# Optimization experiments

Measured on AMD Instinct MI355X. Metric: run time of the kernel, lower is better.

The kernel has to match this reference:

```python
import jax, jax.numpy as jnp
import numpy as np

B = 131072
SD, AD, HID = 24, 8, 32
NH = SD + AD            # n_heads = 32
UNITS = HID * NH        # 1024


def _xavier(k, shape):
    fan_in, fan_out = shape[-2], shape[-1]
    lim = float(np.sqrt(6.0 / (fan_in + fan_out)))
    return jax.random.uniform(k, shape, jnp.float32, -lim, lim)


def setup_inputs() -> dict:
    key = jax.random.key(0)
    ks = jax.random.split(key, 8)
    return dict(
        state=jax.random.normal(ks[0], (B, SD), jnp.float32),
        action=jax.random.normal(ks[1], (B, AD), jnp.float32),
        # ripple layer 1: per-head Linear(NH -> HID), gate logits init 0 (init_prob=0.5)
        W1=_xavier(ks[2], (NH, NH, HID)), b1=jnp.zeros((NH, HID), jnp.float32), g1=jnp.zeros((NH,), jnp.float32),
        # ripple layer 2: per-head Linear(UNITS -> HID)
        W2=_xavier(ks[3], (NH, UNITS, HID)), b2=jnp.zeros((NH, HID), jnp.float32), g2=jnp.zeros((NH,), jnp.float32),
        # q_network
        Wq1=_xavier(ks[4], (UNITS, 256)), bq1=jnp.zeros((256,), jnp.float32),
        ln1_g=jnp.ones((256,), jnp.float32), ln1_b=jnp.zeros((256,), jnp.float32),
        Wq2=_xavier(ks[5], (256, 128)), bq2=jnp.zeros((128,), jnp.float32),
        ln2_g=jnp.ones((128,), jnp.float32), ln2_b=jnp.zeros((128,), jnp.float32),
        Wq3=_xavier(ks[6], (128, 1)), bq3=jnp.zeros((1,), jnp.float32),
    )


def _ripple(x, W, b, g):
    # x: [B, D]; W: [H, D, K]; per-head linear + tanh, scaled by per-head sigmoid gate
    h = jnp.tanh(jnp.einsum('bd,hdk->bhk', x, W) + b[None])  # [B, H, K]
    h = h * jax.nn.sigmoid(g)[None, :, None]
    return h.reshape(x.shape[0], -1)  # [B, H*K]


def _ln(x, g, b, eps=1e-5):
    mu = jnp.mean(x, -1, keepdims=True)
    var = jnp.mean((x - mu) ** 2, -1, keepdims=True)
    return (x - mu) * jax.lax.rsqrt(var + eps) * g + b


def reference(state, action, W1, b1, g1, W2, b2, g2,
              Wq1, bq1, ln1_g, ln1_b, Wq2, bq2, ln2_g, ln2_b, Wq3, bq3):
    sa = jnp.concatenate([state, action], axis=1)          # [B, SD+AD]
    x = _ripple(sa, W1, b1, g1)                            # [B, UNITS]
    x = _ripple(x, W2, b2, g2)                             # [B, UNITS]
    h = jax.nn.relu(_ln(x @ Wq1 + bq1, ln1_g, ln1_b))      # [B, 256] (dropout = eval identity)
    h = jax.nn.relu(_ln(h @ Wq2 + bq2, ln2_g, ln2_b))      # [B, 128]
    return h @ Wq3 + bq3                                   # [B, 1]
```

## Files before the change

### kernel.cpp

```cpp
#include <hip/hip_runtime.h>
#include <hip/hip_bf16.h>

typedef _Float16 f16x8 __attribute__((ext_vector_type(8)));
typedef _Float16 f16x4 __attribute__((ext_vector_type(4)));
typedef float f32x4 __attribute__((ext_vector_type(4)));

__device__ __forceinline__ float tanh_fast(float x) {
  float e = __expf(2.0f * x);
  return 1.0f - 2.0f * __builtin_amdgcn_rcpf(e + 1.0f);
}
__device__ __forceinline__ float sigmoid_fast(float x) {
  return __builtin_amdgcn_rcpf(1.0f + __expf(-x));
}

__global__ __launch_bounds__(256) void prep_weights(
    const float* __restrict__ W1, const float* __restrict__ W2,
    const float* __restrict__ Wq1, const float* __restrict__ Wq2,
    _Float16* __restrict__ V1p, _Float16* __restrict__ V2p,
    _Float16* __restrict__ T1p, _Float16* __restrict__ T2p) {
  __shared__ float S[32 * 33];
  int b = blockIdx.x, t = threadIdx.x;
  if (b < 2624) {
    const float* in; _Float16* out; int N, nc0, tile;
    if (b < 2048) {
      int h = b >> 6, rem = b & 63, ntl = rem >> 5, kt = rem & 31;
      in = W2 + (size_t)h * 32768 + (size_t)kt * 32 * 32;
      N = 32; nc0 = ntl * 16;
      out = V2p; tile = (h * 2 + ntl) * 32 + kt;
    } else if (b < 2560) {
      int i = b - 2048, nt = i >> 5, kt = i & 31;
      in = Wq1 + (size_t)kt * 32 * 256; N = 256; nc0 = nt * 16;
      out = T1p; tile = nt * 32 + kt;
    } else {
      int i = b - 2560, nt = i >> 3, kt = i & 7;
      in = Wq2 + (size_t)kt * 32 * 128; N = 128; nc0 = nt * 16;
      out = T2p; tile = nt * 8 + kt;
    }
    if (t < 128) {
      int r = t >> 2, c4 = (t & 3) * 4;
      const float4 v = *(const float4*)(in + (size_t)r * N + nc0 + c4);
      S[r * 17 + c4 + 0] = v.x; S[r * 17 + c4 + 1] = v.y;
      S[r * 17 + c4 + 2] = v.z; S[r * 17 + c4 + 3] = v.w;
    }
    __syncthreads();
    if (t < 128) {
      int w2 = t >> 6, l = t & 63, q = l >> 4, l15 = l & 15;
      f16x4 o;
#pragma unroll
      for (int jj = 0; jj < 4; ++jj)
        o[jj] = (_Float16)S[(q * 8 + w2 * 4 + jj) * 17 + l15];
      *(f16x4*)(out + (size_t)tile * 512 + l * 8 + w2 * 4) = o;
    }
  } else {
    int h = b - 2624;
    const float* in = W1 + h * 1024;
    int cc = t & 31, rr8 = t >> 5;
#pragma unroll
    for (int p = 0; p < 4; ++p) {
      int r = rr8 + p * 8;
      S[cc * 33 + r] = in[r * 32 + cc];
    }
    __syncthreads();
    if (t < 128) {
      int ntl = t >> 6, l = t & 63, q = l >> 4, l15 = l & 15;
      f16x8 o;
#pragma unroll
      for (int j = 0; j < 8; ++j)
        o[j] = (_Float16)S[(ntl * 16 + l15) * 33 + q * 8 + j];
      *(f16x8*)(V1p + (size_t)(h * 2 + ntl) * 512 + l * 8) = o;
    }
  }
}

__global__ __launch_bounds__(256) void k1_ripple1(
    const float* __restrict__ state, const float* __restrict__ action,
    const _Float16* __restrict__ v1p, const float* __restrict__ b1,
    const float* __restrict__ g1, _Float16* __restrict__ x1p, int gro) {
  __shared__ __align__(16) _Float16 SM[128 * 68];
  int bn = blockIdx.x, bm = blockIdx.y;
  int t = threadIdx.x, w = t >> 6, l = t & 63, q = l >> 4, l15 = l & 15;
  int n0 = bn * 128, m0 = bm * 128;

  {
    int r = t >> 1, half = t & 1;
    size_t grow = (size_t)(gro + m0 + r);
    float v[16];
    if (half == 0) {
      const float4* sp = (const float4*)(state + grow * 24);
      ((float4*)v)[0] = sp[0]; ((float4*)v)[1] = sp[1];
      ((float4*)v)[2] = sp[2]; ((float4*)v)[3] = sp[3];
    } else {
      const float4* sp = (const float4*)(state + grow * 24 + 16);
      ((float4*)v)[0] = sp[0]; ((float4*)v)[1] = sp[1];
      const float4* ap = (const float4*)(action + grow * 8);
      ((float4*)v)[2] = ap[0]; ((float4*)v)[3] = ap[1];
    }
    f16x8 h0, h1;
#pragma unroll
    for (int j = 0; j < 8; ++j) { h0[j] = (_Float16)v[j]; h1[j] = (_Float16)v[8 + j]; }
    *(f16x8*)&SM[r * 40 + half * 16] = h0;
    *(f16x8*)&SM[r * 40 + half * 16 + 8] = h1;
  }
  __syncthreads();

  int wr = w >> 1, wc = w & 1;
  f16x8 af[4], bf[4];
#pragma unroll
  for (int mi = 0; mi < 4; ++mi)
    af[mi] = *(const f16x8*)&SM[(wr * 64 + mi * 16 + l15) * 40 + q * 8];
#pragma unroll
  for (int ni = 0; ni < 4; ++ni)
    bf[ni] = *(const f16x8*)(v1p + (size_t)(bn * 8 + wc * 4 + ni) * 512 + l * 8);

  f32x4 acc[4][4] = {};
#pragma unroll
  for (int mi = 0; mi < 4; ++mi)
#pragma unroll
    for (int ni = 0; ni < 4; ++ni)
      acc[mi][ni] = __builtin_amdgcn_mfma_f32_16x16x32_f16(af[mi], bf[ni], acc[mi][ni], 0, 0, 0);

  for (int p = 0; p < 2; ++p) {
    __syncthreads();
    if (wc == p) {
#pragma unroll
      for (int ni = 0; ni < 4; ++ni) {
        int col = n0 + p * 64 + ni * 16 + l15;
        float sg = sigmoid_fast(g1[col >> 5]);
        float bias = b1[col];
#pragma unroll
        for (int mi = 0; mi < 4; ++mi)
#pragma unroll
          for (int r = 0; r < 4; ++r) {
            int rl = wr * 64 + mi * 16 + q * 4 + r;
            SM[rl * 68 + ni * 16 + l15] = (_Float16)(tanh_fast(acc[mi][ni][r] + bias) * sg);
          }
      }
    }
    __syncthreads();
#pragma unroll
    for (int i = 0; i < 4; ++i) {
      int c = t + i * 256;
      int kcL = c >> 9, rt = (c >> 6) & 7, ll = c & 63;
      int qq = ll >> 4, ll15 = ll & 15;
      int base = (rt * 16 + ll15) * 68 + kcL * 32 + qq * 8;
      union { f16x8 v; f16x4 h[2]; } u;
      u.h[0] = *(const f16x4*)&SM[base];
      u.h[1] = *(const f16x4*)&SM[base + 4];
      *(f16x8*)(x1p + ((size_t)((m0 >> 4) + rt) * 32 + bn * 4 + p * 2 + kcL) * 512 + ll * 8) = u.v;
    }
  }
}

__global__ __launch_bounds__(256, 2) void k2_ripple2(
    const _Float16* __restrict__ x1p, const _Float16* __restrict__ v2p,
    const float* __restrict__ b2, const float* __restrict__ g2,
    _Float16* __restrict__ x2p, int nbm) {
  __shared__ __align__(16) _Float16 EP[4 * 64 * 36];
  int g = blockIdx.x;
  int bn, bm;
  if ((nbm & 7) == 0) {
    int x = g & 7, j = g >> 3;
    bn = j & 3; bm = x + 8 * (j >> 2);
  } else { bn = g & 3; bm = g >> 2; }
  int t = threadIdx.x, w = t >> 6, l = t & 63, q = l >> 4, l15 = l & 15;
  int wr = w >> 1, wc = w & 1;
  int rt0 = bm * 8 + wr * 4;
  int nt0 = bn * 16 + wc * 8;
  f32x4 acc[4][8] = {};

  const _Float16* aB = x1p + (size_t)rt0 * 16384 + l * 8;
  const _Float16* bB = v2p + (size_t)nt0 * 16384 + l * 8;

  f16x8 a0[4], b0[8], a1[4], b1v[8];
#pragma unroll
  for (int mi = 0; mi < 4; ++mi) a0[mi] = *(const f16x8*)(aB + mi * 16384);
#pragma unroll
  for (int ni = 0; ni < 8; ++ni) b0[ni] = *(const f16x8*)(bB + ni * 16384);

  for (int kt = 0; kt < 32; kt += 2) {
#pragma unroll
    for (int mi = 0; mi < 4; ++mi) a1[mi] = *(const f16x8*)(aB + mi * 16384 + (kt + 1) * 512);
#pragma unroll
    for (int ni = 0; ni < 8; ++ni) b1v[ni] = *(const f16x8*)(bB + ni * 16384 + (kt + 1) * 512);
#pragma unroll
    for (int mi = 0; mi < 4; ++mi)
#pragma unroll
      for (int ni = 0; ni < 8; ++ni)
        acc[mi][ni] = __builtin_amdgcn_mfma_f32_16x16x32_f16(a0[mi], b0[ni], acc[mi][ni], 0, 0, 0);
    if (kt + 2 < 32) {
#pragma unroll
      for (int mi = 0; mi < 4; ++mi) a0[mi] = *(const f16x8*)(aB + mi * 16384 + (kt + 2) * 512);
#pragma unroll
      for (int ni = 0; ni < 8; ++ni) b0[ni] = *(const f16x8*)(bB + ni * 16384 + (kt + 2) * 512);
    }
#pragma unroll
    for (int mi = 0; mi < 4; ++mi)
#pragma unroll
      for (int ni = 0; ni < 8; ++ni)
        acc[mi][ni] = __builtin_amdgcn_mfma_f32_16x16x32_f16(a1[mi], b1v[ni], acc[mi][ni], 0, 0, 0);
  }

  _Float16* EPw = EP + w * (64 * 36);
  for (int kcg = 0; kcg < 4; ++kcg) {
#pragma unroll
    for (int np = 0; np < 2; ++np) {
      int ni = kcg * 2 + np;
      int col = (nt0 + ni) * 16 + l15;
      float sg = sigmoid_fast(g2[col >> 5]);
      float bias = b2[col];
#pragma unroll
      for (int mi = 0; mi < 4; ++mi)
#pragma unroll
        for (int r = 0; r < 4; ++r) {
          int row = mi * 16 + q * 4 + r;
          EPw[row * 36 + np * 16 + l15] = (_Float16)(tanh_fast(acc[mi][ni][r] + bias) * sg);
        }
    }
#pragma unroll
    for (int rt = 0; rt < 4; ++rt) {
      int base = (rt * 16 + l15) * 36 + q * 8;
      union { f16x8 v; f16x4 h[2]; } u;
      u.h[0] = *(const f16x4*)&EPw[base];
      u.h[1] = *(const f16x4*)&EPw[base + 4];
      *(f16x8*)(x2p + ((size_t)(rt0 + rt) * 32 + (nt0 >> 1) + kcg) * 512 + l * 8) = u.v;
    }
  }
}

__global__ __launch_bounds__(512, 3) void k3_head(
    const _Float16* __restrict__ x2p, const _Float16* __restrict__ t1p,
    const _Float16* __restrict__ t2p,
    const float* __restrict__ bq1, const float* __restrict__ ln1g, const float* __restrict__ ln1b,
    const float* __restrict__ bq2, const float* __restrict__ ln2g, const float* __restrict__ ln2b,
    const float* __restrict__ wq3, const float* __restrict__ bq3,
    float* __restrict__ out) {
  __shared__ __align__(16) _Float16 y1h[128 * 264];
  __shared__ float redA[128 * 4], redB[128 * 4];
  __shared__ float meanv[128], rstdv[128];
  int bm = blockIdx.x;
  int t = threadIdx.x, w = t >> 6, l = t & 63, q = l >> 4, l15 = l & 15;
  int wr = w >> 2, wc = w & 3;
  int qs_unused = 0; (void)qs_unused;

  f32x4 acc[4][4] = {};
  const _Float16* aB = x2p + (size_t)(bm * 8 + wr * 4) * 16384 + l * 8;
  const _Float16* bB = t1p + (size_t)(wc * 4) * 16384 + l * 8;

  f16x8 a0[4], b0[4], a1[4], b1v[4];
#pragma unroll
  for (int mi = 0; mi < 4; ++mi) a0[mi] = *(const f16x8*)(aB + mi * 16384);
#pragma unroll
  for (int ni = 0; ni < 4; ++ni) b0[ni] = *(const f16x8*)(bB + ni * 16384);

  for (int kt = 0; kt < 32; kt += 2) {
#pragma unroll
    for (int mi = 0; mi < 4; ++mi) a1[mi] = *(const f16x8*)(aB + mi * 16384 + (kt + 1) * 512);
#pragma unroll
    for (int ni = 0; ni < 4; ++ni) b1v[ni] = *(const f16x8*)(bB + ni * 16384 + (kt + 1) * 512);
#pragma unroll
    for (int mi = 0; mi < 4; ++mi)
#pragma unroll
      for (int ni = 0; ni < 4; ++ni)
        acc[mi][ni] = __builtin_amdgcn_mfma_f32_16x16x32_f16(a0[mi], b0[ni], acc[mi][ni], 0, 0, 0);
    if (kt + 2 < 32) {
#pragma unroll
      for (int mi = 0; mi < 4; ++mi) a0[mi] = *(const f16x8*)(aB + mi * 16384 + (kt + 2) * 512);
#pragma unroll
      for (int ni = 0; ni < 4; ++ni) b0[ni] = *(const f16x8*)(bB + ni * 16384 + (kt + 2) * 512);
    }
#pragma unroll
    for (int mi = 0; mi < 4; ++mi)
#pragma unroll
      for (int ni = 0; ni < 4; ++ni)
        acc[mi][ni] = __builtin_amdgcn_mfma_f32_16x16x32_f16(a1[mi], b1v[ni], acc[mi][ni], 0, 0, 0);
  }

#pragma unroll
  for (int ni = 0; ni < 4; ++ni) {
    int col = wc * 64 + ni * 16 + l15;
    float b = bq1[col];
#pragma unroll
    for (int mi = 0; mi < 4; ++mi)
#pragma unroll
      for (int r = 0; r < 4; ++r) acc[mi][ni][r] += b;
  }
#pragma unroll
  for (int mi = 0; mi < 4; ++mi)
#pragma unroll
    for (int r = 0; r < 4; ++r) {
      int row = wr * 64 + mi * 16 + q * 4 + r;
      float s = 0.f, sq = 0.f;
#pragma unroll
      for (int ni = 0; ni < 4; ++ni) { float v = acc[mi][ni][r]; s += v; sq += v * v; }
#pragma unroll
      for (int off = 1; off < 16; off <<= 1) { s += __shfl_xor(s, off); sq += __shfl_xor(sq, off); }
      if (l15 == 0) { redA[row * 4 + wc] = s; redB[row * 4 + wc] = sq; }
    }
  __syncthreads();
  if (t < 128) {
    float s  = redA[t * 4] + redA[t * 4 + 1] + redA[t * 4 + 2] + redA[t * 4 + 3];
    float sq = redB[t * 4] + redB[t * 4 + 1] + redB[t * 4 + 2] + redB[t * 4 + 3];
    float mean = s * (1.0f / 256.0f);
    float var = sq * (1.0f / 256.0f) - mean * mean;
    meanv[t] = mean; rstdv[t] = rsqrtf(var + 1e-5f);
  }
  __syncthreads();
#pragma unroll
  for (int mi = 0; mi < 4; ++mi)
#pragma unroll
    for (int ni = 0; ni < 4; ++ni)
#pragma unroll
      for (int r = 0; r < 4; ++r) {
        int row = wr * 64 + mi * 16 + q * 4 + r;
        int col = wc * 64 + ni * 16 + l15;
        float y = (acc[mi][ni][r] - meanv[row]) * rstdv[row] * ln1g[col] + ln1b[col];
        y = fmaxf(y, 0.f);
        y1h[row * 264 + col] = (_Float16)y;
      }
  __syncthreads();

  f32x4 a2[4][2] = {};
  for (int kt = 0; kt < 8; ++kt) {
    f16x8 af2[4];
#pragma unroll
    for (int mi = 0; mi < 4; ++mi)
      af2[mi] = *(const f16x8*)&y1h[(wr * 64 + mi * 16 + l15) * 264 + kt * 32 + q * 8];
#pragma unroll
    for (int ni = 0; ni < 2; ++ni) {
      f16x8 bf = *(const f16x8*)(t2p + (size_t)(wc * 2 + ni) * 4096 + kt * 512 + l * 8);
#pragma unroll
      for (int mi = 0; mi < 4; ++mi)
        a2[mi][ni] = __builtin_amdgcn_mfma_f32_16x16x32_f16(af2[mi], bf, a2[mi][ni], 0, 0, 0);
    }
  }
#pragma unroll
  for (int ni = 0; ni < 2; ++ni) {
    int col = wc * 32 + ni * 16 + l15;
    float b = bq2[col];
#pragma unroll
    for (int mi = 0; mi < 4; ++mi)
#pragma unroll
      for (int r = 0; r < 4; ++r) a2[mi][ni][r] += b;
  }
  __syncthreads();
#pragma unroll
  for (int mi = 0; mi < 4; ++mi)
#pragma unroll
    for (int r = 0; r < 4; ++r) {
      int row = wr * 64 + mi * 16 + q * 4 + r;
      float s = 0.f, sq = 0.f;
#pragma unroll
      for (int ni = 0; ni < 2; ++ni) { float v = a2[mi][ni][r]; s += v; sq += v * v; }
#pragma unroll
      for (int off = 1; off < 16; off <<= 1) { s += __shfl_xor(s, off); sq += __shfl_xor(sq, off); }
      if (l15 == 0) { redA[row * 4 + wc] = s; redB[row * 4 + wc] = sq; }
    }
  __syncthreads();
  if (t < 128) {
    float s  = redA[t * 4] + redA[t * 4 + 1] + redA[t * 4 + 2] + redA[t * 4 + 3];
    float sq = redB[t * 4] + redB[t * 4 + 1] + redB[t * 4 + 2] + redB[t * 4 + 3];
    float mean = s * (1.0f / 128.0f);
    float var = sq * (1.0f / 128.0f) - mean * mean;
    meanv[t] = mean; rstdv[t] = rsqrtf(var + 1e-5f);
  }
  __syncthreads();
#pragma unroll
  for (int mi = 0; mi < 4; ++mi)
#pragma unroll
    for (int r = 0; r < 4; ++r) {
      int row = wr * 64 + mi * 16 + q * 4 + r;
      float pr = 0.f;
#pragma unroll
      for (int ni = 0; ni < 2; ++ni) {
        int col = wc * 32 + ni * 16 + l15;
        float y = (a2[mi][ni][r] - meanv[row]) * rstdv[row] * ln2g[col] + ln2b[col];
        y = fmaxf(y, 0.f);
        pr += y * wq3[col];
      }
#pragma unroll
      for (int off = 1; off < 16; off <<= 1) pr += __shfl_xor(pr, off);
      if (l15 == 0) redA[row * 4 + wc] = pr;
    }
  __syncthreads();
  if (t < 128)
    out[bm * 128 + t] = redA[t * 4] + redA[t * 4 + 1] + redA[t * 4 + 2] + redA[t * 4 + 3] + bq3[0];
}

extern "C" void kernel_launch(void* const* d_in, const int* in_sizes, int n_in,
                              void* d_out, int out_size, void* d_ws, size_t ws_size,
                              hipStream_t stream) {
  const float* state  = (const float*)d_in[0];
  const float* action = (const float*)d_in[1];
  const float* W1  = (const float*)d_in[2];
  const float* b1  = (const float*)d_in[3];
  const float* g1  = (const float*)d_in[4];
  const float* W2  = (const float*)d_in[5];
  const float* b2  = (const float*)d_in[6];
  const float* g2  = (const float*)d_in[7];
  const float* Wq1 = (const float*)d_in[8];
  const float* bq1 = (const float*)d_in[9];
  const float* ln1g = (const float*)d_in[10];
  const float* ln1b = (const float*)d_in[11];
  const float* Wq2 = (const float*)d_in[12];
  const float* bq2 = (const float*)d_in[13];
  const float* ln2g = (const float*)d_in[14];
  const float* ln2b = (const float*)d_in[15];
  const float* Wq3 = (const float*)d_in[16];
  const float* bq3 = (const float*)d_in[17];
  int B = in_sizes[0] / 24;

  char* ws = (char*)d_ws;
  _Float16* V1p = (_Float16*)(ws);
  _Float16* V2p = (_Float16*)(ws + 65536);
  _Float16* T1p = (_Float16*)(ws + 65536 + 2097152);
  _Float16* T2p = (_Float16*)(ws + 65536 + 2097152 + 524288);
  size_t woff = (65536 + 2097152 + 524288 + 65536 + 4095) & ~(size_t)4095;

  size_t avail = ws_size > woff ? ws_size - woff : 0;
  int S, G;
  if (avail >= (size_t)32768 * 2048 * 3) {
    S = 32768; G = 2;
  } else {
    long rows = (long)(avail / 4096);
    if (rows > 32768) rows = 32768;
    rows &= ~127L;
    if (rows < 128) rows = 128;
    S = (int)rows; G = 1;
  }
  _Float16* x1 = (_Float16*)(ws + woff);
  _Float16* x2 = x1 + (size_t)S * 1024;

  prep_weights<<<2656, 256, 0, stream>>>(W1, W2, Wq1, Wq2, V1p, V2p, T1p, T2p);

  int nsl = (B + S - 1) / S;
  for (int i = 0; i < nsl; ++i) {
    int r0 = i * S;
    int Sc = S < (B - r0) ? S : (B - r0);
    int nbm = Sc / 128;
    k1_ripple1<<<dim3(8, nbm), 256, 0, stream>>>(state, action, V1p, b1, g1, x1, r0);
    k2_ripple2<<<dim3(4 * nbm), 256, 0, stream>>>(x1, V2p, b2, g2,
                                                  x2 + (size_t)(i % G) * S * 1024, nbm);
    if (i % G == G - 1 || i == nsl - 1) {
      int gstart = (i - i % G) * S;
      int nrows = r0 + Sc - gstart;
      k3_head<<<dim3(nrows / 128), 512, 0, stream>>>(x2, T1p, T2p, bq1, ln1g, ln1b,
                                                     bq2, ln2g, ln2b, Wq3, bq3,
                                                     (float*)d_out + gstart);
    }
  }
}
```

Before: 622.5 us.

## Store activation and weight tiles k-major and remap blocks for XCD locality

Changes the packed fp16 layout of x1, x2, V2 and T1 so that tiles for the same k-chunk sit contiguously across row/column tiles, instead of each row tile keeping its full K run together. k1 switches to a 1D grid with an XCD-aware block mapping. k2 walks bm tiles in reverse order, likely so the most recently written x1 rows are read first while still in cache. The GEMM loops are rewritten with pointer strides and a two-stage register prefetch. This targets DRAM/L2 locality and cross-kernel cache reuse, at the cost of larger strides per k-step.

```diff
diff --git a/kernel.cpp b/kernel.cpp
--- a/kernel.cpp
+++ b/kernel.cpp
@@ -26,11 +26,11 @@
       int h = b >> 6, rem = b & 63, ntl = rem >> 5, kt = rem & 31;
       in = W2 + (size_t)h * 32768 + (size_t)kt * 32 * 32;
       N = 32; nc0 = ntl * 16;
-      out = V2p; tile = (h * 2 + ntl) * 32 + kt;
+      out = V2p; tile = kt * 64 + (h * 2 + ntl);
     } else if (b < 2560) {
       int i = b - 2048, nt = i >> 5, kt = i & 31;
       in = Wq1 + (size_t)kt * 32 * 256; N = 256; nc0 = nt * 16;
-      out = T1p; tile = nt * 32 + kt;
+      out = T1p; tile = kt * 16 + nt;
     } else {
       int i = b - 2560, nt = i >> 3, kt = i & 7;
       in = Wq2 + (size_t)kt * 32 * 128; N = 128; nc0 = nt * 16;
@@ -75,9 +75,12 @@
 __global__ __launch_bounds__(256) void k1_ripple1(
     const float* __restrict__ state, const float* __restrict__ action,
     const _Float16* __restrict__ v1p, const float* __restrict__ b1,
-    const float* __restrict__ g1, _Float16* __restrict__ x1p, int gro) {
+    const float* __restrict__ g1, _Float16* __restrict__ x1p, int gro,
+    int NRT, int xcdMatch) {
   __shared__ __align__(16) _Float16 SM[128 * 68];
-  int bn = blockIdx.x, bm = blockIdx.y;
+  int g = blockIdx.x, bn, bm;
+  if (xcdMatch) { int x = g & 7, r = g >> 3; bn = r & 7; bm = x + 8 * (r >> 3); }
+  else { bn = g & 7; bm = g >> 3; }
   int t = threadIdx.x, w = t >> 6, l = t & 63, q = l >> 4, l15 = l & 15;
   int n0 = bn * 128, m0 = bm * 128;
 
@@ -146,7 +149,8 @@
       union { f16x8 v; f16x4 h[2]; } u;
       u.h[0] = *(const f16x4*)&SM[base];
       u.h[1] = *(const f16x4*)&SM[base + 4];
-      *(f16x8*)(x1p + ((size_t)((m0 >> 4) + rt) * 32 + bn * 4 + p * 2 + kcL) * 512 + ll * 8) = u.v;
+      int kc = bn * 4 + p * 2 + kcL;
+      *(f16x8*)(x1p + ((size_t)kc * NRT + (m0 >> 4) + rt) * 512 + ll * 8) = u.v;
     }
   }
 }
@@ -154,13 +158,13 @@
 __global__ __launch_bounds__(256, 2) void k2_ripple2(
     const _Float16* __restrict__ x1p, const _Float16* __restrict__ v2p,
     const float* __restrict__ b2, const float* __restrict__ g2,
-    _Float16* __restrict__ x2p, int nbm) {
+    _Float16* __restrict__ x2p, int nbm, int NRT) {
   __shared__ __align__(16) _Float16 EP[4 * 64 * 36];
   int g = blockIdx.x;
   int bn, bm;
   if ((nbm & 7) == 0) {
-    int x = g & 7, j = g >> 3;
-    bn = j & 3; bm = x + 8 * (j >> 2);
+    int x = g & 7, j = g >> 3, jj = j >> 2, nJ = nbm >> 3;
+    bn = j & 3; bm = x + 8 * (nJ - 1 - jj);
   } else { bn = g & 3; bm = g >> 2; }
   int t = threadIdx.x, w = t >> 6, l = t & 63, q = l >> 4, l15 = l & 15;
   int wr = w >> 1, wc = w & 1;
@@ -168,36 +172,45 @@
   int nt0 = bn * 16 + wc * 8;
   f32x4 acc[4][8] = {};
 
-  const _Float16* aB = x1p + (size_t)rt0 * 16384 + l * 8;
-  const _Float16* bB = v2p + (size_t)nt0 * 16384 + l * 8;
-
-  f16x8 a0[4], b0[8], a1[4], b1v[8];
-#pragma unroll
-  for (int mi = 0; mi < 4; ++mi) a0[mi] = *(const f16x8*)(aB + mi * 16384);
-#pragma unroll
-  for (int ni = 0; ni < 8; ++ni) b0[ni] = *(const f16x8*)(bB + ni * 16384);
+  const size_t aStep = (size_t)NRT * 512;
+  const _Float16* aP = x1p + (size_t)rt0 * 512 + (size_t)l * 8;
+  const _Float16* bP = v2p + (size_t)nt0 * 512 + (size_t)l * 8;
+
+  f16x8 a0[4], a1[4], b0[8], b1[8];
+#pragma unroll
+  for (int mi = 0; mi < 4; ++mi) a0[mi] = *(const f16x8*)(aP + mi * 512);
+#pragma unroll
+  for (int ni = 0; ni < 8; ++ni) b0[ni] = *(const f16x8*)(bP + ni * 512);
+#pragma unroll
+  for (int mi = 0; mi < 4; ++mi) a1[mi] = *(const f16x8*)(aP + aStep + mi * 512);
+#pragma unroll
+  for (int ni = 0; ni < 8; ++ni) b1[ni] = *(const f16x8*)(bP + 32768 + ni * 512);
+  aP += 2 * aStep; bP += 65536;
 
   for (int kt = 0; kt < 32; kt += 2) {
-#pragma unroll
-    for (int mi = 0; mi < 4; ++mi) a1[mi] = *(const f16x8*)(aB + mi * 16384 + (kt + 1) * 512);
-#pragma unroll
-    for (int ni = 0; ni < 8; ++ni) b1v[ni] = *(const f16x8*)(bB + ni * 16384 + (kt + 1) * 512);
 #pragma unroll
     for (int mi = 0; mi < 4; ++mi)
 #pragma unroll
       for (int ni = 0; ni < 8; ++ni)
         acc[mi][ni] = __builtin_amdgcn_mfma_f32_16x16x32_f16(a0[mi], b0[ni], acc[mi][ni], 0, 0, 0);
-    if (kt + 2 < 32) {
-#pragma unroll
-      for (int mi = 0; mi < 4; ++mi) a0[mi] = *(const f16x8*)(aB + mi * 16384 + (kt + 2) * 512);
-#pragma unroll
-      for (int ni = 0; ni < 8; ++ni) b0[ni] = *(const f16x8*)(bB + ni * 16384 + (kt + 2) * 512);
+    if (kt < 30) {
+#pragma unroll
+      for (int mi = 0; mi < 4; ++mi) a0[mi] = *(const f16x8*)(aP + mi * 512);
+#pragma unroll
+      for (int ni = 0; ni < 8; ++ni) b0[ni] = *(const f16x8*)(bP + ni * 512);
     }
 #pragma unroll
     for (int mi = 0; mi < 4; ++mi)
 #pragma unroll
       for (int ni = 0; ni < 8; ++ni)
-        acc[mi][ni] = __builtin_amdgcn_mfma_f32_16x16x32_f16(a1[mi], b1v[ni], acc[mi][ni], 0, 0, 0);
+        acc[mi][ni] = __builtin_amdgcn_mfma_f32_16x16x32_f16(a1[mi], b1[ni], acc[mi][ni], 0, 0, 0);
+    if (kt < 30) {
+#pragma unroll
+      for (int mi = 0; mi < 4; ++mi) a1[mi] = *(const f16x8*)(aP + aStep + mi * 512);
+#pragma unroll
+      for (int ni = 0; ni < 8; ++ni) b1[ni] = *(const f16x8*)(bP + 32768 + ni * 512);
+      aP += 2 * aStep; bP += 65536;
+    }
   }
 
   _Float16* EPw = EP + w * (64 * 36);
@@ -222,7 +235,8 @@
       union { f16x8 v; f16x4 h[2]; } u;
       u.h[0] = *(const f16x4*)&EPw[base];
       u.h[1] = *(const f16x4*)&EPw[base + 4];
-      *(f16x8*)(x2p + ((size_t)(rt0 + rt) * 32 + (nt0 >> 1) + kcg) * 512 + l * 8) = u.v;
+      int kc = (nt0 >> 1) + kcg;
+      *(f16x8*)(x2p + ((size_t)kc * NRT + rt0 + rt) * 512 + l * 8) = u.v;
     }
   }
 }
@@ -233,46 +247,59 @@
     const float* __restrict__ bq1, const float* __restrict__ ln1g, const float* __restrict__ ln1b,
     const float* __restrict__ bq2, const float* __restrict__ ln2g, const float* __restrict__ ln2b,
     const float* __restrict__ wq3, const float* __restrict__ bq3,
-    float* __restrict__ out) {
+    float* __restrict__ out, int NRT, int SROWS) {
   __shared__ __align__(16) _Float16 y1h[128 * 264];
   __shared__ float redA[128 * 4], redB[128 * 4];
   __shared__ float meanv[128], rstdv[128];
   int bm = blockIdx.x;
   int t = threadIdx.x, w = t >> 6, l = t & 63, q = l >> 4, l15 = l & 15;
   int wr = w >> 2, wc = w & 3;
-  int qs_unused = 0; (void)qs_unused;
+
+  int gt = bm * 8;
+  int slice = 0;
+  if (gt >= NRT) { slice = 1; gt -= NRT; }
+  int rt0 = gt + wr * 4;
 
   f32x4 acc[4][4] = {};
-  const _Float16* aB = x2p + (size_t)(bm * 8 + wr * 4) * 16384 + l * 8;
-  const _Float16* bB = t1p + (size_t)(wc * 4) * 16384 + l * 8;
-
-  f16x8 a0[4], b0[4], a1[4], b1v[4];
-#pragma unroll
-  for (int mi = 0; mi < 4; ++mi) a0[mi] = *(const f16x8*)(aB + mi * 16384);
-#pragma unroll
-  for (int ni = 0; ni < 4; ++ni) b0[ni] = *(const f16x8*)(bB + ni * 16384);
+  const size_t aStep = (size_t)NRT * 512;
+  const _Float16* aP = x2p + (size_t)slice * SROWS * 1024 + (size_t)rt0 * 512 + (size_t)l * 8;
+  const _Float16* bP = t1p + (size_t)(wc * 4) * 512 + (size_t)l * 8;
+
+  f16x8 a0[4], a1[4], b0[4], b1[4];
+#pragma unroll
+  for (int mi = 0; mi < 4; ++mi) a0[mi] = *(const f16x8*)(aP + mi * 512);
+#pragma unroll
+  for (int ni = 0; ni < 4; ++ni) b0[ni] = *(const f16x8*)(bP + ni * 512);
+#pragma unroll
+  for (int mi = 0; mi < 4; ++mi) a1[mi] = *(const f16x8*)(aP + aStep + mi * 512);
+#pragma unroll
+  for (int ni = 0; ni < 4; ++ni) b1[ni] = *(const f16x8*)(bP + 8192 + ni * 512);
+  aP += 2 * aStep; bP += 16384;
 
   for (int kt = 0; kt < 32; kt += 2) {
-#pragma unroll
-    for (int mi = 0; mi < 4; ++mi) a1[mi] = *(const f16x8*)(aB + mi * 16384 + (kt + 1) * 512);
-#pragma unroll
-    for (int ni = 0; ni < 4; ++ni) b1v[ni] = *(const f16x8*)(bB + ni * 16384 + (kt + 1) * 512);
 #pragma unroll
     for (int mi = 0; mi < 4; ++mi)
 #pragma unroll
       for (int ni = 0; ni < 4; ++ni)
         acc[mi][ni] = __builtin_amdgcn_mfma_f32_16x16x32_f16(a0[mi], b0[ni], acc[mi][ni], 0, 0, 0);
-    if (kt + 2 < 32) {
-#pragma unroll
-      for (int mi = 0; mi < 4; ++mi) a0[mi] = *(const f16x8*)(aB + mi * 16384 + (kt + 2) * 512);
-#pragma unroll
-      for (int ni = 0; ni < 4; ++ni) b0[ni] = *(const f16x8*)(bB + ni * 16384 + (kt + 2) * 512);
+    if (kt < 30) {
+#pragma unroll
+      for (int mi = 0; mi < 4; ++mi) a0[mi] = *(const f16x8*)(aP + mi * 512);
+#pragma unroll
+      for (int ni = 0; ni < 4; ++ni) b0[ni] = *(const f16x8*)(bP + ni * 512);
     }
 #pragma unroll
     for (int mi = 0; mi < 4; ++mi)
 #pragma unroll
       for (int ni = 0; ni < 4; ++ni)
-        acc[mi][ni] = __builtin_amdgcn_mfma_f32_16x16x32_f16(a1[mi], b1v[ni], acc[mi][ni], 0, 0, 0);
+        acc[mi][ni] = __builtin_amdgcn_mfma_f32_16x16x32_f16(a1[mi], b1[ni], acc[mi][ni], 0, 0, 0);
+    if (kt < 30) {
+#pragma unroll
+      for (int mi = 0; mi < 4; ++mi) a1[mi] = *(const f16x8*)(aP + aStep + mi * 512);
+#pragma unroll
+      for (int ni = 0; ni < 4; ++ni) b1[ni] = *(const f16x8*)(bP + 8192 + ni * 512);
+      aP += 2 * aStep; bP += 16384;
+    }
   }
 
 #pragma unroll
@@ -429,6 +456,7 @@
   }
   _Float16* x1 = (_Float16*)(ws + woff);
   _Float16* x2 = x1 + (size_t)S * 1024;
+  int NRT = S / 16;
 
   prep_weights<<<2656, 256, 0, stream>>>(W1, W2, Wq1, Wq2, V1p, V2p, T1p, T2p);
 
@@ -437,15 +465,17 @@
     int r0 = i * S;
     int Sc = S < (B - r0) ? S : (B - r0);
     int nbm = Sc / 128;
-    k1_ripple1<<<dim3(8, nbm), 256, 0, stream>>>(state, action, V1p, b1, g1, x1, r0);
+    int xm = (nbm & 7) == 0 ? 1 : 0;
+    k1_ripple1<<<dim3(8 * nbm), 256, 0, stream>>>(state, action, V1p, b1, g1, x1, r0,
+                                                  NRT, xm);
     k2_ripple2<<<dim3(4 * nbm), 256, 0, stream>>>(x1, V2p, b2, g2,
-                                                  x2 + (size_t)(i % G) * S * 1024, nbm);
+                                                  x2 + (size_t)(i % G) * S * 1024, nbm, NRT);
     if (i % G == G - 1 || i == nsl - 1) {
       int gstart = (i - i % G) * S;
       int nrows = r0 + Sc - gstart;
       k3_head<<<dim3(nrows / 128), 512, 0, stream>>>(x2, T1p, T2p, bq1, ln1g, ln1b,
                                                      bq2, ln2g, ln2b, Wq3, bq3,
-                                                     (float*)d_out + gstart);
-    }
-  }
-}
+                                                     (float*)d_out + gstart, NRT, S);
+    }
+  }
+}
```

After: 636.7 us. 2.3% more time.
